# Performance work log

Hardware: AMD Instinct MI355X
Metric: run time of the kernel (lower is better)

## Reference

```python
import jax, jax.numpy as jnp
import numpy as np
from jax import lax

# Fixed dims from MSSMamba defaults
B_, L_, DM = 2, 8192, 256
NH, HP, NS = 4, 64, 8          # nheads, headdim, d_state
DIN = NH * HP                  # d_inner = 256
DPROJ = 2 * DIN + 2 * NS + NH  # 532


def setup_inputs() -> dict:
    key = jax.random.key(0)
    ks = jax.random.split(key, 16)
    f = lambda k, s, sc=1.0: jax.random.normal(k, s, jnp.float32) * sc
    inp = {
        'x_H': f(ks[0], (B_, L_, DM)),
        'x_V': f(ks[1], (B_, L_, DM)),
        'W_in_H': f(ks[2], (DM, 2 * DPROJ), 0.05),
        'W_in_V': f(ks[3], (DM, 2 * DPROJ), 0.05),
        'W_out_HF': f(ks[4], (DIN, DM), 0.05),
        'W_out_HB': f(ks[5], (DIN, DM), 0.05),
        'W_out_VF': f(ks[6], (DIN, DM), 0.05),
        'W_out_VB': f(ks[7], (DIN, DM), 0.05),
        'W_out': f(ks[8], (4 * DM, DM), 0.05),
    }
    for i, nm in enumerate(['HF', 'HB', 'VF', 'VB']):
        kd = jax.random.fold_in(ks[9], i)
        ka = jax.random.fold_in(ks[10], i)
        inp['dt_bias_' + nm] = f(kd, (NH,), 0.1)
        inp['A_log_' + nm] = jnp.log(jax.random.uniform(ka, (NH,), jnp.float32, 1.0, 16.0))
        inp['D_' + nm] = jnp.ones((NH,), jnp.float32)
    # per-batch permutation mapping vertical position -> horizontal position
    inp['v2h'] = jax.vmap(lambda k: jax.random.permutation(k, L_))(
        jax.random.split(ks[11], B_)).astype(jnp.int32)
    return inp


def _scan_dir(zxbcdt, dt_bias, A_log, D):
    # zxbcdt: [b, l, DPROJ] -> Mamba2-style selective scan, ngroups=1
    z = zxbcdt[..., :DIN].reshape(B_, L_, NH, HP)
    xBC = jax.nn.silu(zxbcdt[..., DIN:DIN + DIN + 2 * NS])
    x = xBC[..., :DIN].reshape(B_, L_, NH, HP)
    Bm = xBC[..., DIN:DIN + NS]      # [b, l, n]
    Cm = xBC[..., DIN + NS:]         # [b, l, n]
    dt = jax.nn.softplus(zxbcdt[..., -NH:] + dt_bias)  # [b, l, h]
    A = -jnp.exp(A_log)              # [h]
    dA = jnp.exp(dt * A)             # [b, l, h]
    dBx = jnp.einsum('blh,bln,blhp->blhpn', dt, Bm, x)  # [b,l,h,p,n]

    def step(state, inp):
        dA_t, dBx_t, C_t = inp
        state = dA_t[..., None, None] * state + dBx_t   # [b,h,p,n]
        y_t = jnp.einsum('bhpn,bn->bhp', state, C_t)
        return state, y_t

    init = jnp.zeros((B_, NH, HP, NS), dt.dtype)
    _, ys = lax.scan(step, init, (jnp.moveaxis(dA, 1, 0),
                                  jnp.moveaxis(dBx, 1, 0),
                                  jnp.moveaxis(Cm, 1, 0)))
    y = jnp.moveaxis(ys, 0, 1) + D[None, None, :, None] * x  # skip D*x
    y = y * jax.nn.silu(z)                                   # gate
    return y.reshape(B_, L_, DIN)


def reference(x_H, x_V, W_in_H, W_in_V,
              dt_bias_HF, dt_bias_HB, dt_bias_VF, dt_bias_VB,
              A_log_HF, A_log_HB, A_log_VF, A_log_VB,
              D_HF, D_HB, D_VF, D_VB,
              W_out_HF, W_out_HB, W_out_VF, W_out_VB,
              W_out, v2h):
    zx_HF, zx_HB = jnp.split(x_H @ W_in_H, 2, axis=-1)
    zx_VF, zx_VB = jnp.split(x_V @ W_in_V, 2, axis=-1)
    # note: source applies out_proj_HB to the HF branch (kept faithful)
    y_HF = _scan_dir(zx_HF, dt_bias_HF, A_log_HF, D_HF) @ W_out_HB
    y_HB = _scan_dir(zx_HB[:, ::-1], dt_bias_HB, A_log_HB, D_HB)[:, ::-1] @ W_out_HF
    y_VF = _scan_dir(zx_VF, dt_bias_VF, A_log_VF, D_VF) @ W_out_VB
    y_VB = _scan_dir(zx_VB[:, ::-1], dt_bias_VB, A_log_VB, D_VB)[:, ::-1] @ W_out_VF
    # remap vertical-ordered outputs to horizontal ordering (scatter by v2h)
    bidx = jnp.arange(B_)[:, None]
    y_VF = jnp.zeros_like(y_VF).at[bidx, v2h].set(y_VF)
    y_VB = jnp.zeros_like(y_VB).at[bidx, v2h].set(y_VB)
    cat = jnp.concatenate([y_HF, y_HB, y_VF, y_VB], axis=-1)  # [b, l, 4*d_model]
    return jax.nn.silu(cat) @ W_out
```

## Files before the change

### kernel.cpp

```cpp
#include <hip/hip_runtime.h>
#include <hip/hip_bf16.h>

#define B_N 2
#define L_N 8192
#define ROWS 16384
#define CHUNK 32
#define NCHUNK 256
#define GRP 16
#define NGRP 16
#define NPAD 1152

typedef __bf16 bf16x8 __attribute__((ext_vector_type(8)));
typedef float f32x4 __attribute__((ext_vector_type(4)));

__device__ __forceinline__ float siluf(float v) {
  return v * __builtin_amdgcn_rcpf(1.f + __expf(-v));
}
__device__ __forceinline__ float softplusf_(float v) {
  return fmaxf(v, 0.f) + log1pf(__expf(-fabsf(v)));
}
__device__ __forceinline__ unsigned short f2bf(float v) {
  union { __bf16 b; unsigned short u; } x;
  x.b = (__bf16)v;
  return x.u;
}
__device__ __forceinline__ float bf2f(unsigned short u) {
  union { unsigned u; float f; } x; x.u = ((unsigned)u) << 16;
  return x.f;
}

__device__ __forceinline__ void gload_lds16(const unsigned short* g, unsigned short* l) {
  __builtin_amdgcn_global_load_lds(
      (const __attribute__((address_space(1))) unsigned int*)g,
      (__attribute__((address_space(3))) unsigned int*)l, 16, 0, 0);
}

struct P4 { const float* p[4]; };
struct ScanConsts {
  const float* dt_bias[4];
  const float* A_log[4];
  const float* D[4];
};

__global__ __launch_bounds__(256) void k_prep(
    const float* __restrict__ xH, const float* __restrict__ xV,
    const float* __restrict__ WH, const float* __restrict__ WV,
    P4 ws, const float* __restrict__ W_out, const int* __restrict__ v2h, ScanConsts sc,
    unsigned short* __restrict__ xbf, float* __restrict__ dtv_arr, float* __restrict__ dA_arr,
    unsigned short* __restrict__ Wt_in, unsigned short* __restrict__ Wt_dirs,
    unsigned short* __restrict__ Wt_fin, int* __restrict__ inv) {
  __shared__ float xs[32][257];
  __shared__ float Wsm[8][260];
  int bid = blockIdx.x;
  int tid = threadIdx.x;
  if (bid < 1024) {
    const int mat = bid >> 9;
    const float* x = mat ? xV : xH;
    const float* W = mat ? WV : WH;
    const int r0 = (bid & 511) * 32;
    for (int i = tid; i < 2048; i += 256) {
      int c = i >> 8, k = i & 255;
      int sl = c >> 2, h = c & 3;
      Wsm[c][k] = W[(long)k * 1064 + sl * 532 + 528 + h];
    }
    for (int i = tid; i < 32 * 64; i += 256) {
      int rl = i >> 6, kq = (i & 63) * 4;
      float4 v = *(const float4*)(x + (long)(r0 + rl) * 256 + kq);
      xs[rl][kq + 0] = v.x; xs[rl][kq + 1] = v.y; xs[rl][kq + 2] = v.z; xs[rl][kq + 3] = v.w;
    }
    __syncthreads();
    for (int i = tid; i < 32 * 64; i += 256) {
      int rl = i >> 6, kq = (i & 63) * 4;
      ushort4 o;
      o.x = f2bf(xs[rl][kq + 0]);
      o.y = f2bf(xs[rl][kq + 1]);
      o.z = f2bf(xs[rl][kq + 2]);
      o.w = f2bf(xs[rl][kq + 3]);
      *(ushort4*)(xbf + (size_t)mat * ROWS * 256 + (long)(r0 + rl) * 256 + kq) = o;
    }
    const int rl = tid >> 3, c = tid & 7;
    float s = 0.f;
    #pragma unroll 8
    for (int k = 0; k < 256; ++k) s = fmaf(xs[rl][k], Wsm[c][k], s);
    const int sl = c >> 2, h = c & 3;
    const int dir = mat * 2 + sl;
    float dtv = softplusf_(s + sc.dt_bias[dir][h]);
    float dAv = __expf(dtv * (-__expf(sc.A_log[dir][h])));
    long o = ((long)dir * 4 + h) * ROWS + (r0 + rl);
    dtv_arr[o] = dtv;
    dA_arr[o] = dAv;
  } else if (bid < 3328) {
    int i = (bid - 1024) * 256 + tid;
    int z = i / (NPAD * 256);
    int rem = i - z * (NPAD * 256);
    int n = rem >> 8, k = rem & 255;
    const float* W = z ? WV : WH;
    int sl = n >= 544;
    int cc = n - (sl ? 544 : 0);
    float v = (cc < 532) ? W[(long)k * 1064 + sl * 532 + cc] : 0.f;
    Wt_in[i] = f2bf(v);
  } else if (bid < 4352) {
    int i = (bid - 3328) * 256 + tid;
    int d = i >> 16;
    int rem = i & 65535;
    int n = rem >> 8, k = rem & 255;
    Wt_dirs[i] = f2bf(ws.p[d][(long)k * 256 + n]);
  } else if (bid < 5376) {
    int i = (bid - 4352) * 256 + tid;
    int n = i >> 10, k = i & 1023;
    Wt_fin[i] = f2bf(W_out[(long)k * 256 + n]);
  } else {
    int m = (bid - 5376) * 256 + tid;
    if (m < ROWS) {
      int b = m >> 13;
      inv[b * L_N + v2h[m]] = m;
    }
  }
}

struct EpiIn {
  unsigned short* zraw;
  unsigned short* xraw;
  unsigned short* bc;
};

__global__ __launch_bounds__(256) void k_gemm_in(
    const unsigned short* __restrict__ Abase, const unsigned short* __restrict__ Btbase,
    EpiIn ep) {
  __shared__ unsigned short smem[24576];
  const int tid = threadIdx.x;
  const int lane = tid & 63;
  const int wid = tid >> 6;
  const int wm = wid & 1, wn = wid >> 1;
  const int q = lane >> 4, r = lane & 15;
  const int m0 = blockIdx.x * 128;
  const int n0 = blockIdx.y * 128;
  const int z = blockIdx.z;
  const unsigned short* A = Abase + (long)z * ROWS * 256;
  const unsigned short* Bt = Btbase + (long)z * NPAD * 256;

  int s_row[2], s_ch[2];
  #pragma unroll
  for (int i = 0; i < 2; ++i) {
    int idx = i * 256 + tid;
    s_row[i] = idx >> 2;
    s_ch[i] = (idx & 3) ^ ((s_row[i] >> 1) & 3);
  }

  auto stage = [&](int ti) {
    const int slot = ti % 3;
    const int kt = ti * 32;
    #pragma unroll
    for (int i = 0; i < 2; ++i) {
      gload_lds16(A + (long)(m0 + s_row[i]) * 256 + kt + s_ch[i] * 8,
                  smem + (size_t)slot * 4096 + (size_t)(i * 256 + wid * 64) * 8);
      gload_lds16(Bt + (long)(n0 + s_row[i]) * 256 + kt + s_ch[i] * 8,
                  smem + 12288 + (size_t)slot * 4096 + (size_t)(i * 256 + wid * 64) * 8);
    }
  };

  f32x4 acc[4][4] = {};
  const int swr = (r >> 1) & 3;

  stage(0);
  stage(1);

  #pragma unroll
  for (int i = 0; i < 8; ++i) {
    if (i < 7) asm volatile("s_waitcnt vmcnt(4)" ::: "memory");
    else       asm volatile("s_waitcnt vmcnt(0)" ::: "memory");
    __builtin_amdgcn_s_barrier();
    __builtin_amdgcn_sched_barrier(0);
    if (i + 2 < 8) stage(i + 2);
    const int slot = i % 3;
    bf16x8 af[4], bfr[4];
    #pragma unroll
    for (int mi = 0; mi < 4; ++mi)
      af[mi] = *(const bf16x8*)&smem[(size_t)slot * 4096 +
                                     ((wm * 64 + mi * 16 + r) * 4 + (q ^ swr)) * 8];
    #pragma unroll
    for (int ni = 0; ni < 4; ++ni)
      bfr[ni] = *(const bf16x8*)&smem[12288 + (size_t)slot * 4096 +
                                      ((wn * 64 + ni * 16 + r) * 4 + (q ^ swr)) * 8];
    __builtin_amdgcn_s_setprio(1);
    #pragma unroll
    for (int mi = 0; mi < 4; ++mi)
      #pragma unroll
      for (int ni = 0; ni < 4; ++ni)
        acc[mi][ni] = __builtin_amdgcn_mfma_f32_16x16x32_bf16(af[mi], bfr[ni], acc[mi][ni], 0, 0, 0);
    __builtin_amdgcn_s_setprio(0);
  }
  __syncthreads();

  unsigned short* tr = smem + wid * (16 * 72);
  #pragma unroll
  for (int mi = 0; mi < 4; ++mi) {
    #pragma unroll
    for (int ni = 0; ni < 4; ++ni)
      #pragma unroll
      for (int j = 0; j < 4; ++j)
        tr[(q * 4 + j) * 72 + ni * 16 + r] = f2bf(acc[mi][ni][j]);
    asm volatile("s_waitcnt lgkmcnt(0)" ::: "memory");
    #pragma unroll
    for (int pass = 0; pass < 2; ++pass) {
      int rl = pass * 8 + (lane >> 3);
      int c8 = (lane & 7) * 8;
      bf16x8 v = *(const bf16x8*)&tr[rl * 72 + c8];
      int row = m0 + wm * 64 + mi * 16 + rl;
      int col = n0 + wn * 64 + c8;
      int sl = col >= 544;
      int cc = col - (sl ? 544 : 0);
      if (cc < 528) {
        int dir = z * 2 + sl;
        if (cc < 256)
          *(bf16x8*)(ep.zraw + ((long)dir * ROWS + row) * 256 + cc) = v;
        else if (cc < 512)
          *(bf16x8*)(ep.xraw + ((long)dir * ROWS + row) * 256 + cc - 256) = v;
        else
          *(bf16x8*)(ep.bc + ((long)dir * ROWS + row) * 16 + cc - 512) = v;
      }
    }
    asm volatile("s_waitcnt lgkmcnt(0)" ::: "memory");
  }
}

__global__ __launch_bounds__(512) void k_fuse(
    const unsigned short* __restrict__ ybf,
    const unsigned short* __restrict__ Wt_dirs,
    const unsigned short* __restrict__ Wt_fin,
    unsigned short* __restrict__ pbuf) {
  __shared__ unsigned short smf[47616];
  unsigned short* Ab = smf;
  unsigned short* Bb = smf + 6144;
  unsigned short* Tl = smf + 30720;
  const int tid = threadIdx.x;
  const int lane = tid & 63;
  const int wid = tid >> 6;
  const int wm = wid & 1, wn = wid >> 1;
  const int q = lane >> 4, r = lane & 15;
  const int r0 = blockIdx.x * 64;
  const int pair = blockIdx.y;
  const int swr = (r >> 1) & 3;

  const int a_row = tid >> 2;
  const int a_ch = (tid & 3) ^ ((a_row >> 1) & 3);
  const long a_off = (long)(r0 + a_row) * 256 + a_ch * 8;
  int b_row[2], b_ch[2];
  #pragma unroll
  for (int rnd = 0; rnd < 2; ++rnd) {
    int idx = rnd * 512 + tid;
    b_row[rnd] = idx >> 2;
    b_ch[rnd] = (idx & 3) ^ ((b_row[rnd] >> 1) & 3);
  }

  auto stageT = [&](int g) {
    const int seg = g >> 3, ti = g & 7, kt = ti * 32;
    const int dl = pair * 2 + (seg >> 1);
    const int slot = g % 3;
    if ((seg & 1) == 0) {
      if (tid < 256)
        gload_lds16(ybf + (long)dl * ROWS * 256 + a_off + kt,
                    Ab + (size_t)slot * 2048 + (size_t)(wid * 64) * 8);
      #pragma unroll
      for (int rnd = 0; rnd < 2; ++rnd)
        gload_lds16(Wt_dirs + (long)dl * 65536 + (long)b_row[rnd] * 256 + kt + b_ch[rnd] * 8,
                    Bb + (size_t)slot * 8192 + (size_t)(rnd * 512 + wid * 64) * 8);
    } else {
      #pragma unroll
      for (int rnd = 0; rnd < 2; ++rnd)
        gload_lds16(Wt_fin + (long)b_row[rnd] * 1024 + dl * 256 + kt + b_ch[rnd] * 8,
                    Bb + (size_t)slot * 8192 + (size_t)(rnd * 512 + wid * 64) * 8);
    }
  };

  f32x4 acc_o[2][4] = {};

  stageT(0);
  stageT(1);

  #pragma unroll
  for (int dd = 0; dd < 2; ++dd) {
    f32x4 acc_t[2][4] = {};
    #pragma unroll
    for (int i = 0; i < 8; ++i) {
      const int g = dd * 16 + i;
      asm volatile("s_waitcnt vmcnt(2)" ::: "memory");
      __builtin_amdgcn_s_barrier();
      __builtin_amdgcn_sched_barrier(0);
      stageT(g + 2);
      const int slot = g % 3;
      bf16x8 af[2], bfr[4];
      #pragma unroll
      for (int mi = 0; mi < 2; ++mi)
        af[mi] = *(const bf16x8*)&Ab[(size_t)slot * 2048 +
                                     ((wm * 32 + mi * 16 + r) * 4 + (q ^ swr)) * 8];
      #pragma unroll
      for (int ni = 0; ni < 4; ++ni)
        bfr[ni] = *(const bf16x8*)&Bb[(size_t)slot * 8192 +
                                      ((wn * 64 + ni * 16 + r) * 4 + (q ^ swr)) * 8];
      __builtin_amdgcn_s_setprio(1);
      #pragma unroll
      for (int mi = 0; mi < 2; ++mi)
        #pragma unroll
        for (int ni = 0; ni < 4; ++ni)
          acc_t[mi][ni] = __builtin_amdgcn_mfma_f32_16x16x32_bf16(af[mi], bfr[ni], acc_t[mi][ni], 0, 0, 0);
      __builtin_amdgcn_s_setprio(0);
    }
    #pragma unroll
    for (int mi = 0; mi < 2; ++mi)
      #pragma unroll
      for (int ni = 0; ni < 4; ++ni)
        #pragma unroll
        for (int j = 0; j < 4; ++j)
          Tl[(wm * 32 + mi * 16 + q * 4 + j) * 264 + wn * 64 + ni * 16 + r] =
              f2bf(siluf(acc_t[mi][ni][j]));
    asm volatile("s_waitcnt lgkmcnt(0)" ::: "memory");
    #pragma unroll
    for (int i = 0; i < 8; ++i) {
      const int g = dd * 16 + 8 + i;
      if (g < 31) asm volatile("s_waitcnt vmcnt(2)" ::: "memory");
      else        asm volatile("s_waitcnt vmcnt(0)" ::: "memory");
      __builtin_amdgcn_s_barrier();
      __builtin_amdgcn_sched_barrier(0);
      if (g + 2 < 32) stageT(g + 2);
      const int slot = g % 3;
      const int kt = i * 32;
      bf16x8 af[2], bfr[4];
      #pragma unroll
      for (int mi = 0; mi < 2; ++mi)
        af[mi] = *(const bf16x8*)&Tl[(wm * 32 + mi * 16 + r) * 264 + kt + q * 8];
      #pragma unroll
      for (int ni = 0; ni < 4; ++ni)
        bfr[ni] = *(const bf16x8*)&Bb[(size_t)slot * 8192 +
                                      ((wn * 64 + ni * 16 + r) * 4 + (q ^ swr)) * 8];
      __builtin_amdgcn_s_setprio(1);
      #pragma unroll
      for (int mi = 0; mi < 2; ++mi)
        #pragma unroll
        for (int ni = 0; ni < 4; ++ni)
          acc_o[mi][ni] = __builtin_amdgcn_mfma_f32_16x16x32_bf16(af[mi], bfr[ni], acc_o[mi][ni], 0, 0, 0);
      __builtin_amdgcn_s_setprio(0);
    }
  }

  __syncthreads();
  #pragma unroll
  for (int mi = 0; mi < 2; ++mi)
    #pragma unroll
    for (int ni = 0; ni < 4; ++ni)
      #pragma unroll
      for (int j = 0; j < 4; ++j)
        Tl[(wm * 32 + mi * 16 + q * 4 + j) * 264 + wn * 64 + ni * 16 + r] = f2bf(acc_o[mi][ni][j]);
  __syncthreads();
  unsigned short* pout = pbuf + (long)pair * ROWS * 256;
  #pragma unroll
  for (int pass = 0; pass < 4; ++pass) {
    int id = pass * 512 + tid;
    int row = id >> 5, c8 = (id & 31) * 8;
    bf16x8 v = *(const bf16x8*)&Tl[row * 264 + c8];
    *(bf16x8*)(pout + (long)(r0 + row) * 256 + c8) = v;
  }
}

__global__ void k_red(const unsigned short* __restrict__ pbuf,
                      const int* __restrict__ inv, float* __restrict__ out) {
  int i = blockIdx.x * 256 + threadIdx.x;
  int row = i >> 5, c8 = (i & 31) * 8;
  uint4 a = *(const uint4*)(pbuf + (long)row * 256 + c8);
  int vrow = inv[row];
  uint4 b = *(const uint4*)(pbuf + (size_t)ROWS * 256 + (long)vrow * 256 + c8);
  const unsigned short* au = (const unsigned short*)&a;
  const unsigned short* bu = (const unsigned short*)&b;
  float rr[8];
  #pragma unroll
  for (int j = 0; j < 8; ++j) rr[j] = bf2f(au[j]) + bf2f(bu[j]);
  ((float4*)out)[i * 2] = *(float4*)&rr[0];
  ((float4*)out)[i * 2 + 1] = *(float4*)&rr[4];
}

struct ScanP {
  const unsigned short* xraw;
  const unsigned short* zraw;
  const unsigned short* bc;
  const float* dtv;
  const float* dA;
  const float* D[4];
};

__global__ __launch_bounds__(64) void k_scan1(ScanP sp, float* __restrict__ S,
                                              float* __restrict__ P) {
  __shared__ __align__(16) float Bst[CHUNK][8];
  __shared__ float dAs[CHUNK];
  const int p = threadIdx.x;
  const int c = blockIdx.x;
  const int bh = blockIdx.y;
  const int d = blockIdx.z;
  const int b = bh >> 2, h = bh & 3;
  const int rev = d & 1;
  const int t0 = c * CHUNK;
  if (p < CHUNK) {
    const int t = t0 + p;
    const int l = rev ? (L_N - 1 - t) : t;
    const int row = (b << 13) + l;
    uint4 bv = *(const uint4*)(sp.bc + ((long)d * ROWS + row) * 16);
    const unsigned short* bu = (const unsigned short*)&bv;
    float dtvv = sp.dtv[((long)d * 4 + h) * ROWS + row];
    dAs[p] = sp.dA[((long)d * 4 + h) * ROWS + row];
    #pragma unroll
    for (int n = 0; n < 8; ++n) Bst[p][n] = siluf(bf2f(bu[n])) * dtvv;
  }
  __syncthreads();

  float st[8] = {0, 0, 0, 0, 0, 0, 0, 0};
  float cumdA = 1.f;
  const int l0 = rev ? (L_N - 1 - t0) : t0;
  const unsigned short* xp = sp.xraw + ((long)d * ROWS + (b << 13) + l0) * 256 + h * 64 + p;
  const long stp = rev ? -256L : 256L;

  unsigned short xa[8], xb[8];
  #pragma unroll
  for (int j = 0; j < 8; ++j) xa[j] = xp[(long)j * stp];
  #pragma unroll
  for (int g = 0; g < 4; ++g) {
    if (g < 3) {
      #pragma unroll
      for (int j = 0; j < 8; ++j) xb[j] = xp[(long)((g + 1) * 8 + j) * stp];
    }
    #pragma unroll
    for (int j = 0; j < 8; ++j) {
      int s = g * 8 + j;
      float x = siluf(bf2f(xa[j]));
      float dA = dAs[s];
      f32x4 B0 = *(const f32x4*)&Bst[s][0];
      f32x4 B1 = *(const f32x4*)&Bst[s][4];
      cumdA *= dA;
      st[0] = fmaf(dA, st[0], x * B0[0]);
      st[1] = fmaf(dA, st[1], x * B0[1]);
      st[2] = fmaf(dA, st[2], x * B0[2]);
      st[3] = fmaf(dA, st[3], x * B0[3]);
      st[4] = fmaf(dA, st[4], x * B1[0]);
      st[5] = fmaf(dA, st[5], x * B1[1]);
      st[6] = fmaf(dA, st[6], x * B1[2]);
      st[7] = fmaf(dA, st[7], x * B1[3]);
    }
    #pragma unroll
    for (int j = 0; j < 8; ++j) xa[j] = xb[j];
  }
  float* Sp = S + ((((long)d * NCHUNK + c) * 8 + bh) * 64 + p) * 8;
  #pragma unroll
  for (int n = 0; n < 8; ++n) Sp[n] = st[n];
  if (p == 0) P[((long)d * NCHUNK + c) * 8 + bh] = cumdA;
}

__global__ __launch_bounds__(512) void k_scan2a(const float* __restrict__ S,
                                                const float* __restrict__ P,
                                                float* __restrict__ carry_loc,
                                                float* __restrict__ Sg,
                                                float* __restrict__ Pg) {
  __shared__ float Pl[GRP];
  const int tid = threadIdx.x;
  const int gid = blockIdx.x;
  const int g = gid & 15;
  const int dbh = gid >> 4;
  const int d = dbh >> 3, bh = dbh & 7;
  if (tid < GRP) Pl[tid] = P[((long)d * NCHUNK + g * GRP + tid) * 8 + bh];
  __syncthreads();
  float cy = 0.f;
  #pragma unroll
  for (int i = 0; i < GRP; ++i) {
    const int c = g * GRP + i;
    carry_loc[(((long)d * NCHUNK + c) * 8 + bh) * 512 + tid] = cy;
    const float Sv = S[(((long)d * NCHUNK + c) * 8 + bh) * 512 + tid];
    cy = fmaf(Pl[i], cy, Sv);
  }
  Sg[(((long)d * NGRP + g) * 8 + bh) * 512 + tid] = cy;
  if (tid == 0) {
    float pp = 1.f;
    #pragma unroll
    for (int i = 0; i < GRP; ++i) pp *= Pl[i];
    Pg[((long)d * NGRP + g) * 8 + bh] = pp;
  }
}

__global__ __launch_bounds__(512) void k_scan2b(const float* __restrict__ Sg,
                                                const float* __restrict__ Pg,
                                                float* __restrict__ gcarry) {
  __shared__ float Pgl[NGRP];
  const int tid = threadIdx.x;
  const int dbh = blockIdx.x;
  const int d = dbh >> 3, bh = dbh & 7;
  if (tid < NGRP) Pgl[tid] = Pg[((long)d * NGRP + tid) * 8 + bh];
  __syncthreads();
  float cy = 0.f;
  #pragma unroll
  for (int g = 0; g < NGRP; ++g) {
    gcarry[(((long)d * NGRP + g) * 8 + bh) * 512 + tid] = cy;
    const float Sv = Sg[(((long)d * NGRP + g) * 8 + bh) * 512 + tid];
    cy = fmaf(Pgl[g], cy, Sv);
  }
}

__global__ __launch_bounds__(64) void k_scan3(ScanP sp,
                                              const float* __restrict__ carry_loc,
                                              const float* __restrict__ gcarry,
                                              const float* __restrict__ Pc,
                                              unsigned short* __restrict__ ybf) {
  __shared__ __align__(16) float Bst[CHUNK][8];
  __shared__ __align__(16) float Cst[CHUNK][8];
  __shared__ float dAs[CHUNK];
  __shared__ float Pgr[GRP];
  const int p = threadIdx.x;
  const int c = blockIdx.x;
  const int bh = blockIdx.y;
  const int d = blockIdx.z;
  const int b = bh >> 2, h = bh & 3;
  const int rev = d & 1;
  const float Dv = sp.D[d][h];
  const int t0 = c * CHUNK;
  const int grp = c >> 4, ii = c & 15;
  if (p < ii) Pgr[p] = Pc[((long)d * NCHUNK + grp * GRP + p) * 8 + bh];
  if (p < CHUNK) {
    const int t = t0 + p;
    const int l = rev ? (L_N - 1 - t) : t;
    const int row = (b << 13) + l;
    const unsigned short* bp = sp.bc + ((long)d * ROWS + row) * 16;
    uint4 bv = *(const uint4*)bp;
    uint4 cv = *(const uint4*)(bp + 8);
    const unsigned short* bu = (const unsigned short*)&bv;
    const unsigned short* cu = (const unsigned short*)&cv;
    float dtvv = sp.dtv[((long)d * 4 + h) * ROWS + row];
    dAs[p] = sp.dA[((long)d * 4 + h) * ROWS + row];
    #pragma unroll
    for (int n = 0; n < 8; ++n) Bst[p][n] = siluf(bf2f(bu[n])) * dtvv;
    #pragma unroll
    for (int n = 0; n < 8; ++n) Cst[p][n] = siluf(bf2f(cu[n]));
  }
  __syncthreads();

  float pref = 1.f;
  for (int k = 0; k < ii; ++k) pref *= Pgr[k];
  float st[8];
  {
    const float* clp = carry_loc + ((((long)d * NCHUNK + c) * 8 + bh) * 64 + p) * 8;
    const float* gcp = gcarry + ((((long)d * NGRP + grp) * 8 + bh) * 64 + p) * 8;
    #pragma unroll
    for (int n = 0; n < 8; ++n) st[n] = fmaf(pref, gcp[n], clp[n]);
  }

  const int l0 = rev ? (L_N - 1 - t0) : t0;
  const long base = (long)(b << 13) + l0;
  const unsigned short* xp = sp.xraw + ((long)d * ROWS + base) * 256 + h * 64 + p;
  const unsigned short* zp = sp.zraw + ((long)d * ROWS + base) * 256 + h * 64 + p;
  unsigned short* yp = ybf + ((long)d * ROWS + base) * 256 + h * 64 + p;
  const long stp = rev ? -256L : 256L;

  unsigned short xa[8], xb[8], za[8], zb[8];
  #pragma unroll
  for (int j = 0; j < 8; ++j) { xa[j] = xp[(long)j * stp]; za[j] = zp[(long)j * stp]; }
  #pragma unroll
  for (int g = 0; g < 4; ++g) {
    if (g < 3) {
      #pragma unroll
      for (int j = 0; j < 8; ++j) {
        xb[j] = xp[(long)((g + 1) * 8 + j) * stp];
        zb[j] = zp[(long)((g + 1) * 8 + j) * stp];
      }
    }
    #pragma unroll
    for (int j = 0; j < 8; ++j) {
      int s = g * 8 + j;
      float x = siluf(bf2f(xa[j]));
      float zv = siluf(bf2f(za[j]));
      float dA = dAs[s];
      f32x4 B0 = *(const f32x4*)&Bst[s][0];
      f32x4 B1 = *(const f32x4*)&Bst[s][4];
      f32x4 C0 = *(const f32x4*)&Cst[s][0];
      f32x4 C1 = *(const f32x4*)&Cst[s][4];
      st[0] = fmaf(dA, st[0], x * B0[0]);
      st[1] = fmaf(dA, st[1], x * B0[1]);
      st[2] = fmaf(dA, st[2], x * B0[2]);
      st[3] = fmaf(dA, st[3], x * B0[3]);
      st[4] = fmaf(dA, st[4], x * B1[0]);
      st[5] = fmaf(dA, st[5], x * B1[1]);
      st[6] = fmaf(dA, st[6], x * B1[2]);
      st[7] = fmaf(dA, st[7], x * B1[3]);
      float y01 = fmaf(st[1], C0[1], st[0] * C0[0]);
      float y23 = fmaf(st[3], C0[3], st[2] * C0[2]);
      float y45 = fmaf(st[5], C1[1], st[4] * C1[0]);
      float y67 = fmaf(st[7], C1[3], st[6] * C1[2]);
      float y = (y01 + y23) + (y45 + y67);
      y = fmaf(Dv, x, y) * zv;
      yp[(long)s * stp] = f2bf(y);
    }
    #pragma unroll
    for (int j = 0; j < 8; ++j) { xa[j] = xb[j]; za[j] = zb[j]; }
  }
}

extern "C" void kernel_launch(void* const* d_in, const int* in_sizes, int n_in,
                              void* d_out, int out_size, void* d_ws, size_t ws_size,
                              hipStream_t stream) {
  const float* x_H = (const float*)d_in[0];
  const float* x_V = (const float*)d_in[1];
  const float* W_in_H = (const float*)d_in[2];
  const float* W_in_V = (const float*)d_in[3];
  const float* W_out_HF = (const float*)d_in[4];
  const float* W_out_HB = (const float*)d_in[5];
  const float* W_out_VF = (const float*)d_in[6];
  const float* W_out_VB = (const float*)d_in[7];
  const float* W_out = (const float*)d_in[8];
  const float* dt_bias_HF = (const float*)d_in[9];
  const float* A_log_HF = (const float*)d_in[10];
  const float* D_HF = (const float*)d_in[11];
  const float* dt_bias_HB = (const float*)d_in[12];
  const float* A_log_HB = (const float*)d_in[13];
  const float* D_HB = (const float*)d_in[14];
  const float* dt_bias_VF = (const float*)d_in[15];
  const float* A_log_VF = (const float*)d_in[16];
  const float* D_VF = (const float*)d_in[17];
  const float* dt_bias_VB = (const float*)d_in[18];
  const float* A_log_VB = (const float*)d_in[19];
  const float* D_VB = (const float*)d_in[20];
  const int* v2h = (const int*)d_in[21];

  char* ws = (char*)d_ws;
  size_t off = 0;
  auto alloc = [&](size_t bytes) {
    void* pp = ws + off;
    off = (off + bytes + 255) & ~(size_t)255;
    return pp;
  };
  unsigned short* xbf = (unsigned short*)alloc((size_t)2 * ROWS * 256 * 2);
  unsigned short* Wt_in = (unsigned short*)alloc((size_t)2 * NPAD * 256 * 2);
  unsigned short* Wt_dirs = (unsigned short*)alloc((size_t)4 * 65536 * 2);
  unsigned short* Wt_fin = (unsigned short*)alloc((size_t)256 * 1024 * 2);
  unsigned short* zraw = (unsigned short*)alloc((size_t)4 * ROWS * 256 * 2);
  unsigned short* xraw = (unsigned short*)alloc((size_t)4 * ROWS * 256 * 2);
  unsigned short* bc = (unsigned short*)alloc((size_t)4 * ROWS * 16 * 2);
  float* dtv_arr = (float*)alloc((size_t)16 * ROWS * 4);
  float* dA_arr = (float*)alloc((size_t)16 * ROWS * 4);
  unsigned short* ybf = (unsigned short*)alloc((size_t)4 * ROWS * 256 * 2);
  float* S = (float*)alloc((size_t)4 * NCHUNK * 8 * 512 * 4);
  float* P = (float*)alloc((size_t)4 * NCHUNK * 8 * 4);
  float* carry_loc = (float*)alloc((size_t)4 * NCHUNK * 8 * 512 * 4);
  float* Sg = (float*)alloc((size_t)4 * NGRP * 8 * 512 * 4);
  float* Pg = (float*)alloc((size_t)4 * NGRP * 8 * 4);
  float* gcarry = (float*)alloc((size_t)4 * NGRP * 8 * 512 * 4);
  int* inv = (int*)alloc((size_t)ROWS * 4);
  unsigned short* pbuf = (unsigned short*)alloc((size_t)2 * ROWS * 256 * 2);

  ScanConsts sc;
  sc.dt_bias[0] = dt_bias_HF; sc.dt_bias[1] = dt_bias_HB;
  sc.dt_bias[2] = dt_bias_VF; sc.dt_bias[3] = dt_bias_VB;
  sc.A_log[0] = A_log_HF; sc.A_log[1] = A_log_HB;
  sc.A_log[2] = A_log_VF; sc.A_log[3] = A_log_VB;
  sc.D[0] = D_HF; sc.D[1] = D_HB; sc.D[2] = D_VF; sc.D[3] = D_VB;

  P4 wdirs;
  wdirs.p[0] = W_out_HB; wdirs.p[1] = W_out_HF; wdirs.p[2] = W_out_VB; wdirs.p[3] = W_out_VF;

  k_prep<<<5440, 256, 0, stream>>>(x_H, x_V, W_in_H, W_in_V, wdirs, W_out, v2h, sc,
                                   xbf, dtv_arr, dA_arr, Wt_in, Wt_dirs, Wt_fin, inv);

  EpiIn ep; ep.zraw = zraw; ep.xraw = xraw; ep.bc = bc;

  k_gemm_in<<<dim3(ROWS / 128, NPAD / 128, 2), 256, 0, stream>>>(xbf, Wt_in, ep);

  ScanP sp;
  sp.xraw = xraw; sp.zraw = zraw; sp.bc = bc; sp.dtv = dtv_arr; sp.dA = dA_arr;
  sp.D[0] = D_HF; sp.D[1] = D_HB; sp.D[2] = D_VF; sp.D[3] = D_VB;

  k_scan1<<<dim3(NCHUNK, 8, 4), 64, 0, stream>>>(sp, S, P);
  k_scan2a<<<512, 512, 0, stream>>>(S, P, carry_loc, Sg, Pg);
  k_scan2b<<<32, 512, 0, stream>>>(Sg, Pg, gcarry);
  k_scan3<<<dim3(NCHUNK, 8, 4), 64, 0, stream>>>(sp, carry_loc, gcarry, P, ybf);

  k_fuse<<<dim3(ROWS / 64, 2), 512, 0, stream>>>(ybf, Wt_dirs, Wt_fin, pbuf);
  k_red<<<ROWS * 256 / 8 / 256, 256, 0, stream>>>(pbuf, inv, (float*)d_out);

  (void)in_sizes; (void)n_in; (void)out_size; (void)ws_size;
}
```

Before: 251.6 us.

## Fuse vertical-row gather and final reduction into k_fuse, drop k_red

k_fuse now processes all four directions per 64-row block, gathering the vertical-direction rows of ybf through the inverse permutation inside the A-tile load. It accumulates the full output in registers and writes fp32 directly to the output, which removes the bf16 partial buffer, the separate reduction kernel and one launch. The cost is that the grid shrinks from 512 blocks to 256, each with twice the serial K loop, so fewer blocks are available to fill the GPU's compute units. The vertical A-tile loads also become row-scattered.

New measurement: 240.6 us. 4.4% less time.

```diff
diff --git a/kernel.cpp b/kernel.cpp
--- a/kernel.cpp
+++ b/kernel.cpp
@@ -228,23 +228,26 @@
     const unsigned short* __restrict__ ybf,
     const unsigned short* __restrict__ Wt_dirs,
     const unsigned short* __restrict__ Wt_fin,
-    unsigned short* __restrict__ pbuf) {
+    const int* __restrict__ inv,
+    float* __restrict__ out) {
   __shared__ unsigned short smf[47616];
   unsigned short* Ab = smf;
   unsigned short* Bb = smf + 6144;
   unsigned short* Tl = smf + 30720;
+  float* Ttmp = (float*)(smf + 30720);
   const int tid = threadIdx.x;
   const int lane = tid & 63;
   const int wid = tid >> 6;
   const int wm = wid & 1, wn = wid >> 1;
   const int q = lane >> 4, r = lane & 15;
   const int r0 = blockIdx.x * 64;
-  const int pair = blockIdx.y;
   const int swr = (r >> 1) & 3;
 
   const int a_row = tid >> 2;
   const int a_ch = (tid & 3) ^ ((a_row >> 1) & 3);
-  const long a_off = (long)(r0 + a_row) * 256 + a_ch * 8;
+  const long a_offH = (long)(r0 + a_row) * 256 + a_ch * 8;
+  long a_offV = 0;
+  if (tid < 256) a_offV = (long)inv[r0 + a_row] * 256 + a_ch * 8;
   int b_row[2], b_ch[2];
   #pragma unroll
   for (int rnd = 0; rnd < 2; ++rnd) {
@@ -255,11 +258,12 @@
 
   auto stageT = [&](int g) {
     const int seg = g >> 3, ti = g & 7, kt = ti * 32;
-    const int dl = pair * 2 + (seg >> 1);
+    const int dl = seg >> 1;
     const int slot = g % 3;
     if ((seg & 1) == 0) {
+      const long aoff = (dl >= 2) ? a_offV : a_offH;
       if (tid < 256)
-        gload_lds16(ybf + (long)dl * ROWS * 256 + a_off + kt,
+        gload_lds16(ybf + (long)dl * ROWS * 256 + aoff + kt,
                     Ab + (size_t)slot * 2048 + (size_t)(wid * 64) * 8);
       #pragma unroll
       for (int rnd = 0; rnd < 2; ++rnd)
@@ -279,11 +283,11 @@
   stageT(1);
 
   #pragma unroll
-  for (int dd = 0; dd < 2; ++dd) {
+  for (int d = 0; d < 4; ++d) {
     f32x4 acc_t[2][4] = {};
     #pragma unroll
     for (int i = 0; i < 8; ++i) {
-      const int g = dd * 16 + i;
+      const int g = d * 16 + i;
       asm volatile("s_waitcnt vmcnt(2)" ::: "memory");
       __builtin_amdgcn_s_barrier();
       __builtin_amdgcn_sched_barrier(0);
@@ -317,12 +321,12 @@
     asm volatile("s_waitcnt lgkmcnt(0)" ::: "memory");
     #pragma unroll
     for (int i = 0; i < 8; ++i) {
-      const int g = dd * 16 + 8 + i;
-      if (g < 31) asm volatile("s_waitcnt vmcnt(2)" ::: "memory");
+      const int g = d * 16 + 8 + i;
+      if (g < 63) asm volatile("s_waitcnt vmcnt(2)" ::: "memory");
       else        asm volatile("s_waitcnt vmcnt(0)" ::: "memory");
       __builtin_amdgcn_s_barrier();
       __builtin_amdgcn_sched_barrier(0);
-      if (g + 2 < 32) stageT(g + 2);
+      if (g + 2 < 64) stageT(g + 2);
       const int slot = g % 3;
       const int kt = i * 32;
       bf16x8 af[2], bfr[4];
@@ -345,37 +349,26 @@
 
   __syncthreads();
   #pragma unroll
-  for (int mi = 0; mi < 2; ++mi)
-    #pragma unroll
-    for (int ni = 0; ni < 4; ++ni)
-      #pragma unroll
-      for (int j = 0; j < 4; ++j)
-        Tl[(wm * 32 + mi * 16 + q * 4 + j) * 264 + wn * 64 + ni * 16 + r] = f2bf(acc_o[mi][ni][j]);
-  __syncthreads();
-  unsigned short* pout = pbuf + (long)pair * ROWS * 256;
-  #pragma unroll
-  for (int pass = 0; pass < 4; ++pass) {
-    int id = pass * 512 + tid;
-    int row = id >> 5, c8 = (id & 31) * 8;
-    bf16x8 v = *(const bf16x8*)&Tl[row * 264 + c8];
-    *(bf16x8*)(pout + (long)(r0 + row) * 256 + c8) = v;
-  }
-}
-
-__global__ void k_red(const unsigned short* __restrict__ pbuf,
-                      const int* __restrict__ inv, float* __restrict__ out) {
-  int i = blockIdx.x * 256 + threadIdx.x;
-  int row = i >> 5, c8 = (i & 31) * 8;
-  uint4 a = *(const uint4*)(pbuf + (long)row * 256 + c8);
-  int vrow = inv[row];
-  uint4 b = *(const uint4*)(pbuf + (size_t)ROWS * 256 + (long)vrow * 256 + c8);
-  const unsigned short* au = (const unsigned short*)&a;
-  const unsigned short* bu = (const unsigned short*)&b;
-  float rr[8];
-  #pragma unroll
-  for (int j = 0; j < 8; ++j) rr[j] = bf2f(au[j]) + bf2f(bu[j]);
-  ((float4*)out)[i * 2] = *(float4*)&rr[0];
-  ((float4*)out)[i * 2 + 1] = *(float4*)&rr[4];
+  for (int h = 0; h < 2; ++h) {
+    if (wm == h) {
+      #pragma unroll
+      for (int mi = 0; mi < 2; ++mi)
+        #pragma unroll
+        for (int ni = 0; ni < 4; ++ni)
+          #pragma unroll
+          for (int j = 0; j < 4; ++j)
+            Ttmp[(mi * 16 + q * 4 + j) * 260 + wn * 64 + ni * 16 + r] = acc_o[mi][ni][j];
+    }
+    __syncthreads();
+    #pragma unroll
+    for (int pass = 0; pass < 4; ++pass) {
+      int id = pass * 512 + tid;
+      int row = id >> 6, c4 = (id & 63) * 4;
+      float4 v = *(const float4*)&Ttmp[row * 260 + c4];
+      *(float4*)(out + (long)(r0 + h * 32 + row) * 256 + c4) = v;
+    }
+    if (h == 0) __syncthreads();
+  }
 }
 
 struct ScanP {
@@ -647,7 +640,6 @@
   float* Pg = (float*)alloc((size_t)4 * NGRP * 8 * 4);
   float* gcarry = (float*)alloc((size_t)4 * NGRP * 8 * 512 * 4);
   int* inv = (int*)alloc((size_t)ROWS * 4);
-  unsigned short* pbuf = (unsigned short*)alloc((size_t)2 * ROWS * 256 * 2);
 
   ScanConsts sc;
   sc.dt_bias[0] = dt_bias_HF; sc.dt_bias[1] = dt_bias_HB;
@@ -675,8 +667,7 @@
   k_scan2b<<<32, 512, 0, stream>>>(Sg, Pg, gcarry);
   k_scan3<<<dim3(NCHUNK, 8, 4), 64, 0, stream>>>(sp, carry_loc, gcarry, P, ybf);
 
-  k_fuse<<<dim3(ROWS / 64, 2), 512, 0, stream>>>(ybf, Wt_dirs, Wt_fin, pbuf);
-  k_red<<<ROWS * 256 / 8 / 256, 256, 0, stream>>>(pbuf, inv, (float*)d_out);
+  k_fuse<<<256, 512, 0, stream>>>(ybf, Wt_dirs, Wt_fin, inv, (float*)d_out);
 
   (void)in_sizes; (void)n_in; (void)out_size; (void)ws_size;
 }
```
